# Optimization experiments

Hardware: AMD Instinct MI355X
Metric: run time of the kernel (lower is better)

The kernel has to match this reference:

```python
import jax, jax.numpy as jnp
import numpy as np

DIM, HEADS = 1024, 16
HEAD_DIM = DIM // HEADS
SCALE = HEAD_DIM ** -0.5


def setup_inputs() -> dict:
    key = jax.random.key(0)
    ks = jax.random.split(key, 5)
    B, N = 2, 2048
    x = jax.random.normal(ks[0], (B, N, DIM), dtype=jnp.float32)
    freqs = jax.random.normal(ks[1], (N, HEAD_DIM // 2), dtype=jnp.float32)
    w_qkv = jax.random.normal(ks[2], (3 * DIM, DIM), dtype=jnp.float32) * 0.02
    w_proj = jax.random.normal(ks[3], (DIM, DIM), dtype=jnp.float32) * 0.02
    b_proj = jnp.zeros((DIM,), dtype=jnp.float32)
    return {"x": x, "freqs": freqs, "w_qkv": w_qkv, "w_proj": w_proj, "b_proj": b_proj}


def _apply_rotary(t, cos, sin):
    # t: (B,N,H,D); cos/sin: (1,N,1,D//2)
    B, N, H, D = t.shape
    tp = t.reshape(B, N, H, D // 2, 2)
    x1, x2 = tp[..., 0], tp[..., 1]
    out = jnp.stack([x1 * cos - x2 * sin, x1 * sin + x2 * cos], axis=-1)
    return out.reshape(B, N, H, D)


def reference(x, freqs, w_qkv, w_proj, b_proj):
    B, N, C = x.shape
    H, D = HEADS, HEAD_DIM
    qkv = (x @ w_qkv.T).reshape(B, N, 3, H, D)  # fused QKV projection
    q, k, v = qkv[:, :, 0], qkv[:, :, 1], qkv[:, :, 2]  # each (B,N,H,D)
    cos = jnp.cos(freqs)[None, :, None, :]  # (1,N,1,D/2)
    sin = jnp.sin(freqs)[None, :, None, :]
    q = _apply_rotary(q, cos, sin)
    k = _apply_rotary(k, cos, sin)
    # SDPA: scores (B,H,N,N)
    scores = jnp.einsum("bqhd,bkhd->bhqk", q, k) * SCALE
    attn = jax.nn.softmax(scores, axis=-1)
    out = jnp.einsum("bhqk,bkhd->bqhd", attn, v).reshape(B, N, C)
    return out @ w_proj.T + b_proj
```

## Files before the change

### kernel.cpp

```cpp
#include <hip/hip_runtime.h>
#include <hip/hip_bf16.h>
#include <stdint.h>

#define BATCH   2
#define SEQ     2048
#define CDIM    1024
#define NHEAD   16
#define HDIM    64
#define MROWS   (BATCH*SEQ)
#define QKVN    (3*CDIM)
#define ATT_SCALE 0.125f

typedef __hip_bfloat16 bf16;
using bf16x8 = __attribute__((ext_vector_type(8))) __bf16;
using f32x4  = __attribute__((ext_vector_type(4))) float;

__device__ __forceinline__ void gld16(const void* g, void* l) {
    __builtin_amdgcn_global_load_lds(
        (__attribute__((address_space(1))) void*)(void*)(g),
        (__attribute__((address_space(3))) void*)(l),
        16, 0, 0);
}

__device__ __forceinline__ f32x4 mfma16x16x32(bf16x8 a, bf16x8 b, f32x4 c) {
    return __builtin_amdgcn_mfma_f32_16x16x32_bf16(a, b, c, 0, 0, 0);
}

__device__ __forceinline__ uint16_t bfbits(float v) {
    bf16 b = __float2bfloat16(v);
    return *(uint16_t*)&b;
}
__device__ __forceinline__ void store_out(bf16* p, float v) { *p = __float2bfloat16(v); }
__device__ __forceinline__ void store_out(float* p, float v) { *p = v; }

#define NX_F4 ((size_t)MROWS*CDIM/4)
#define NQ_F4 ((size_t)QKVN*CDIM/4)
#define NP_F4 ((size_t)CDIM*CDIM/4)
#define NF_SC ((size_t)SEQ*32)

__global__ __launch_bounds__(256)
void cvt_kernel(const float* __restrict__ x, const float* __restrict__ wq,
                const float* __restrict__ wp, const float* __restrict__ freqs,
                bf16* __restrict__ xb, bf16* __restrict__ wqb,
                bf16* __restrict__ wpb, float2* __restrict__ csn) {
    size_t i4 = (size_t)blockIdx.x*256 + threadIdx.x;
    if (i4 < NX_F4 + NQ_F4 + NP_F4) {
        const float* src; bf16* dst; size_t off;
        if (i4 < NX_F4)           { src = x;  dst = xb;  off = i4; }
        else if (i4 < NX_F4+NQ_F4){ src = wq; dst = wqb; off = i4 - NX_F4; }
        else                      { src = wp; dst = wpb; off = i4 - NX_F4 - NQ_F4; }
        float4 v = ((const float4*)src)[off];
        bf16 o[4] = { __float2bfloat16(v.x), __float2bfloat16(v.y),
                      __float2bfloat16(v.z), __float2bfloat16(v.w) };
        *(uint64_t*)(dst + off*4) = *(const uint64_t*)o;
    } else if (i4 < NX_F4 + NQ_F4 + NP_F4 + NF_SC) {
        size_t k = i4 - (NX_F4 + NQ_F4 + NP_F4);
        float f = freqs[k];
        csn[k] = make_float2(cosf(f), sinf(f));
    }
}

__global__ __launch_bounds__(256)
void gemm_qkv_rope(const bf16* __restrict__ A, const bf16* __restrict__ Bw,
                   const float2* __restrict__ csn, bf16* __restrict__ Qr,
                   bf16* __restrict__ Kr, bf16* __restrict__ VT) {
    const int K = CDIM, N = QKVN;
    __shared__ __align__(16) bf16 sh[64*136];
    bf16* As = sh;
    bf16* Bs = sh + 4096;

    const int bm = blockIdx.x, bn = blockIdx.y;
    const int tid  = threadIdx.x;
    const int lane = tid & 63;
    const int w    = tid >> 6;
    const int wm   = (w & 1) * 64;
    const int wn   = (w >> 1) * 64;
    const int quad = lane >> 4;
    const int l16  = lane & 15;

    const int c0 = tid, c1 = tid + 256;
    const size_t a_off0 = (size_t)(bm*128 + (c0 >> 2)) * K + (c0 & 3) * 8;
    const size_t a_off1 = (size_t)(bm*128 + (c1 >> 2)) * K + (c1 & 3) * 8;
    const size_t b_off0 = (size_t)(bn*128 + (c0 >> 2)) * K + (c0 & 3) * 8;
    const size_t b_off1 = (size_t)(bn*128 + (c1 >> 2)) * K + (c1 & 3) * 8;

    f32x4 acc[4][4] = {};

    for (int k0 = 0; k0 < K; k0 += 32) {
        __syncthreads();
        gld16(A + a_off0 + k0, &As[c0*8]);
        gld16(A + a_off1 + k0, &As[c1*8]);
        gld16(Bw + b_off0 + k0, &Bs[c0*8]);
        gld16(Bw + b_off1 + k0, &Bs[c1*8]);
        __syncthreads();

        bf16x8 af[4], bfv[4];
#pragma unroll
        for (int i = 0; i < 4; i++)
            af[i] = *(const bf16x8*)&As[(wm + i*16 + l16)*32 + quad*8];
#pragma unroll
        for (int i = 0; i < 4; i++)
            bfv[i] = *(const bf16x8*)&Bs[(wn + i*16 + l16)*32 + quad*8];
#pragma unroll
        for (int mi = 0; mi < 4; mi++)
#pragma unroll
            for (int ni = 0; ni < 4; ni++)
                acc[mi][ni] = mfma16x16x32(af[mi], bfv[ni], acc[mi][ni]);
    }

    const int region = bn >> 3;
    if (region < 2) {
        bf16* dst = region ? Kr : Qr;
        const int odd = l16 & 1;
#pragma unroll
        for (int mi = 0; mi < 4; mi++) {
#pragma unroll
            for (int ni = 0; ni < 4; ni++) {
                const int cq = (bn & 7)*128 + wn + ni*16 + l16;
                const int h = cq >> 6, d = cq & 63, fi = d >> 1;
#pragma unroll
                for (int r = 0; r < 4; r++) {
                    const int m = bm*128 + wm + mi*16 + quad*4 + r;
                    const int bb = m >> 11, n = m & 2047;
                    float own = acc[mi][ni][r];
                    float prt = __shfl_xor(own, 1);
                    float2 cs2 = csn[n*32 + fi];
                    float o = odd ? (prt*cs2.y + own*cs2.x)
                                  : (own*cs2.x - prt*cs2.y);
                    dst[((size_t)(bb*16 + h)*SEQ + n)*HDIM + d] = __float2bfloat16(o);
                }
            }
        }
    } else {
        const int bb = (bm*128) >> 11, n0 = (bm*128) & 2047;
        __syncthreads();
#pragma unroll
        for (int cc = 0; cc < 2; ++cc) {
            if ((w >> 1) == cc) {
#pragma unroll
                for (int mi = 0; mi < 4; mi++)
#pragma unroll
                    for (int ni = 0; ni < 4; ni++) {
                        const int d  = ni*16 + l16;
                        const int nl = wm + mi*16 + quad*4;
                        uint2 pk;
                        pk.x = (uint32_t)bfbits(acc[mi][ni][0]) |
                               ((uint32_t)bfbits(acc[mi][ni][1]) << 16);
                        pk.y = (uint32_t)bfbits(acc[mi][ni][2]) |
                               ((uint32_t)bfbits(acc[mi][ni][3]) << 16);
                        *(uint2*)&sh[d*136 + nl] = pk;
                    }
            }
            __syncthreads();
            const int h = (bn - 16)*2 + cc;
            const int d = tid >> 2, tn = tid & 3;
            bf16* vdst = VT + ((size_t)(bb*16 + h)*HDIM + d)*SEQ + n0 + tn*32;
#pragma unroll
            for (int j = 0; j < 4; j++)
                *(uint4*)(vdst + j*8) = *(const uint4*)&sh[d*136 + tn*32 + j*8];
            __syncthreads();
        }
    }
}

template<typename OutT, bool ADD_BIAS>
__global__ __launch_bounds__(256)
void gemm_bt(const bf16* __restrict__ A, const bf16* __restrict__ Bw,
             const float* __restrict__ bias, OutT* __restrict__ C,
             int M, int N, int K) {
    __shared__ __align__(16) bf16 As[128*32];
    __shared__ __align__(16) bf16 Bs[128*32];

    const int bm = blockIdx.x, bn = blockIdx.y;
    const int tid  = threadIdx.x;
    const int lane = tid & 63;
    const int w    = tid >> 6;
    const int wm   = (w & 1) * 64;
    const int wn   = (w >> 1) * 64;
    const int quad = lane >> 4;
    const int l16  = lane & 15;

    const int c0 = tid, c1 = tid + 256;
    const size_t a_off0 = (size_t)(bm*128 + (c0 >> 2)) * K + (c0 & 3) * 8;
    const size_t a_off1 = (size_t)(bm*128 + (c1 >> 2)) * K + (c1 & 3) * 8;
    const size_t b_off0 = (size_t)(bn*128 + (c0 >> 2)) * K + (c0 & 3) * 8;
    const size_t b_off1 = (size_t)(bn*128 + (c1 >> 2)) * K + (c1 & 3) * 8;

    f32x4 acc[4][4] = {};

    for (int k0 = 0; k0 < K; k0 += 32) {
        __syncthreads();
        gld16(A + a_off0 + k0, &As[c0*8]);
        gld16(A + a_off1 + k0, &As[c1*8]);
        gld16(Bw + b_off0 + k0, &Bs[c0*8]);
        gld16(Bw + b_off1 + k0, &Bs[c1*8]);
        __syncthreads();

        bf16x8 af[4], bfv[4];
#pragma unroll
        for (int i = 0; i < 4; i++)
            af[i] = *(const bf16x8*)&As[(wm + i*16 + l16)*32 + quad*8];
#pragma unroll
        for (int i = 0; i < 4; i++)
            bfv[i] = *(const bf16x8*)&Bs[(wn + i*16 + l16)*32 + quad*8];
#pragma unroll
        for (int mi = 0; mi < 4; mi++)
#pragma unroll
            for (int ni = 0; ni < 4; ni++)
                acc[mi][ni] = mfma16x16x32(af[mi], bfv[ni], acc[mi][ni]);
    }

#pragma unroll
    for (int mi = 0; mi < 4; mi++) {
        const int r0 = bm*128 + wm + mi*16 + quad*4;
#pragma unroll
        for (int ni = 0; ni < 4; ni++) {
            const int c = bn*128 + wn + ni*16 + l16;
            float bv = 0.f;
            if (ADD_BIAS) bv = bias[c];
#pragma unroll
            for (int r = 0; r < 4; r++)
                store_out(&C[(size_t)(r0 + r)*N + c], acc[mi][ni][r] + bv);
        }
    }
}

#define PSTRIDE 72

__global__ __launch_bounds__(256)
void attn_kernel(const bf16* __restrict__ Qr, const bf16* __restrict__ Kr,
                 const bf16* __restrict__ VT, bf16* __restrict__ Ao) {
    const int blk = blockIdx.x;
    const int bh  = blk >> 4;
    const int b   = bh >> 4, h = bh & 15;
    const int q0  = (blk & 15) * 128;
    const int tid = threadIdx.x;
    const int w   = tid >> 6, lane = tid & 63;
    const int quad = lane >> 4, l16 = lane & 15;

    __shared__ __align__(16) bf16 Ks[2][64*64];
    __shared__ __align__(16) bf16 Vs[2][64*64];
    __shared__ __align__(16) bf16 Ps[4][2*16*PSTRIDE];

    bf16x8 qf[2][2];
#pragma unroll
    for (int t = 0; t < 2; t++) {
        const int qrow = q0 + w*32 + t*16 + l16;
        const bf16* qp = Qr + ((size_t)bh*SEQ + qrow)*HDIM + quad*8;
        qf[t][0] = *(const bf16x8*)(qp);
        qf[t][1] = *(const bf16x8*)(qp + 32);
    }

    const int s0 = tid, s1 = tid + 256;
    const int r0 = s0 >> 3, g0 = (s0 & 7) ^ (r0 & 7);
    const int r1 = s1 >> 3, g1 = (s1 & 7) ^ (r1 & 7);
    const bf16* kb0 = Kr + (size_t)bh*SEQ*HDIM + r0*HDIM + g0*8;
    const bf16* kb1 = Kr + (size_t)bh*SEQ*HDIM + r1*HDIM + g1*8;
    const bf16* vb0 = VT + (size_t)bh*HDIM*SEQ + r0*SEQ + g0*8;
    const bf16* vb1 = VT + (size_t)bh*HDIM*SEQ + r1*SEQ + g1*8;

    f32x4 acc[2][4] = {};
    float lsum[2] = {0.f, 0.f};

    gld16(kb0, &Ks[0][s0*8]);
    gld16(kb1, &Ks[0][s1*8]);
    gld16(vb0, &Vs[0][s0*8]);
    gld16(vb1, &Vs[0][s1*8]);

    const int swz = l16 & 7;

    for (int it = 0; it < SEQ/64; ++it) {
        const int cur = it & 1, nxt = cur ^ 1;
        __syncthreads();
        if (it + 1 < SEQ/64) {
            const size_t ko = (size_t)(it + 1) * 64 * HDIM;
            const size_t vo = (size_t)(it + 1) * 64;
            gld16(kb0 + ko, &Ks[nxt][s0*8]);
            gld16(kb1 + ko, &Ks[nxt][s1*8]);
            gld16(vb0 + vo, &Vs[nxt][s0*8]);
            gld16(vb1 + vo, &Vs[nxt][s1*8]);
        }

        f32x4 sv[2][4];
#pragma unroll
        for (int j = 0; j < 4; j++) {
            const bf16* krow = &Ks[cur][(j*16 + l16)*64];
            bf16x8 ka = *(const bf16x8*)(krow + ((quad     ^ swz) * 8));
            bf16x8 kb = *(const bf16x8*)(krow + (((quad+4) ^ swz) * 8));
#pragma unroll
            for (int t = 0; t < 2; t++) {
                f32x4 tacc = {};
                tacc = mfma16x16x32(ka, qf[t][0], tacc);
                tacc = mfma16x16x32(kb, qf[t][1], tacc);
                sv[t][j] = tacc;
            }
        }

#pragma unroll
        for (int t = 0; t < 2; t++) {
#pragma unroll
            for (int j = 0; j < 4; j++) {
                float e0 = __expf(sv[t][j][0] * ATT_SCALE);
                float e1 = __expf(sv[t][j][1] * ATT_SCALE);
                float e2 = __expf(sv[t][j][2] * ATT_SCALE);
                float e3 = __expf(sv[t][j][3] * ATT_SCALE);
                lsum[t] += (e0 + e1) + (e2 + e3);
                uint2 pk;
                pk.x = (uint32_t)bfbits(e0) | ((uint32_t)bfbits(e1) << 16);
                pk.y = (uint32_t)bfbits(e2) | ((uint32_t)bfbits(e3) << 16);
                *(uint2*)&Ps[w][(t*16 + l16)*PSTRIDE + j*16 + quad*4] = pk;
            }
        }
        asm volatile("s_waitcnt lgkmcnt(0)" ::: "memory");

        bf16x8 pf[2][2];
#pragma unroll
        for (int t = 0; t < 2; t++) {
            const bf16* pr = &Ps[w][(t*16 + l16)*PSTRIDE + quad*8];
            pf[t][0] = *(const bf16x8*)(pr);
            pf[t][1] = *(const bf16x8*)(pr + 32);
        }
#pragma unroll
        for (int dt = 0; dt < 4; dt++) {
            const bf16* vrow = &Vs[cur][(dt*16 + l16)*64];
            bf16x8 va = *(const bf16x8*)(vrow + ((quad     ^ swz) * 8));
            bf16x8 vb = *(const bf16x8*)(vrow + (((quad+4) ^ swz) * 8));
#pragma unroll
            for (int t = 0; t < 2; t++) {
                acc[t][dt] = mfma16x16x32(pf[t][0], va, acc[t][dt]);
                acc[t][dt] = mfma16x16x32(pf[t][1], vb, acc[t][dt]);
            }
        }
    }

#pragma unroll
    for (int t = 0; t < 2; t++) {
        lsum[t] += __shfl_xor(lsum[t], 16, 64);
        lsum[t] += __shfl_xor(lsum[t], 32, 64);
    }
    float lt[2][4];
#pragma unroll
    for (int t = 0; t < 2; t++)
#pragma unroll
        for (int r = 0; r < 4; r++)
            lt[t][r] = __shfl(lsum[t], quad*20 + r, 64);

#pragma unroll
    for (int t = 0; t < 2; t++)
#pragma unroll
        for (int dt = 0; dt < 4; dt++)
#pragma unroll
            for (int r = 0; r < 4; r++) {
                int qr  = q0 + w*32 + t*16 + quad*4 + r;
                int col = h*HDIM + dt*16 + l16;
                Ao[(size_t)(b*SEQ + qr)*CDIM + col] =
                    __float2bfloat16(acc[t][dt][r] / lt[t][r]);
            }
}

extern "C" void kernel_launch(void* const* d_in, const int* in_sizes, int n_in,
                              void* d_out, int out_size, void* d_ws, size_t ws_size,
                              hipStream_t stream) {
    const float* x      = (const float*)d_in[0];
    const float* freqs  = (const float*)d_in[1];
    const float* w_qkv  = (const float*)d_in[2];
    const float* w_proj = (const float*)d_in[3];
    const float* b_proj = (const float*)d_in[4];
    float* out = (float*)d_out;

    char* ws = (char*)d_ws;
    bf16*   xb    = (bf16*)ws;   ws += (size_t)MROWS * CDIM * sizeof(bf16);
    bf16*   wqkvb = (bf16*)ws;   ws += (size_t)QKVN * CDIM * sizeof(bf16);
    bf16*   wprojb= (bf16*)ws;   ws += (size_t)CDIM * CDIM * sizeof(bf16);
    float2* csn   = (float2*)ws; ws += (size_t)SEQ * 32 * sizeof(float2);
    bf16*   Qr    = (bf16*)ws;   ws += (size_t)BATCH*NHEAD*SEQ*HDIM*sizeof(bf16);
    bf16*   Kr    = (bf16*)ws;   ws += (size_t)BATCH*NHEAD*SEQ*HDIM*sizeof(bf16);
    bf16*   VT    = (bf16*)ws;   ws += (size_t)BATCH*NHEAD*SEQ*HDIM*sizeof(bf16);
    bf16*   Ao    = (bf16*)ws;

    dim3 blk(256);
    {
        size_t nthr = NX_F4 + NQ_F4 + NP_F4 + NF_SC;
        cvt_kernel<<<dim3((nthr + 255) / 256), blk, 0, stream>>>(
            x, w_qkv, w_proj, freqs, xb, wqkvb, wprojb, csn);
    }
    gemm_qkv_rope<<<dim3(MROWS/128, QKVN/128), blk, 0, stream>>>(
        xb, wqkvb, csn, Qr, Kr, VT);
    attn_kernel<<<dim3(BATCH*NHEAD*(SEQ/128)), blk, 0, stream>>>(
        Qr, Kr, VT, Ao);
    gemm_bt<float, true><<<dim3(MROWS/128, CDIM/128), blk, 0, stream>>>(
        Ao, wprojb, b_proj, out, MROWS, CDIM, CDIM);
}
```

Measured before the change: 221.5 us.

## Keep softmax P in registers via 16x16x16 MFMA with pre-tiled V layout

The QKV GEMM epilogue now writes V in a fragment-tiled layout matching the 16x16x16 bf16 MFMA B-operand. This lets the attention kernel feed exponentiated scores straight from registers into the PV MFMAs instead of round-tripping P through shared memory. The softmax scale and log2(e) are folded into Q at projection time so exp2 can be used directly, and bf16 packing uses a cheap rounding bit trick. The trade-offs are twice as many (smaller) MFMA instructions for PV and a slightly different rounding scheme.

```diff
diff --git a/kernel.cpp b/kernel.cpp
--- a/kernel.cpp
+++ b/kernel.cpp
@@ -9,11 +9,12 @@
 #define HDIM    64
 #define MROWS   (BATCH*SEQ)
 #define QKVN    (3*CDIM)
-#define ATT_SCALE 0.125f
+#define QSCALE  0.18033688011112042f
 
 typedef __hip_bfloat16 bf16;
 using bf16x8 = __attribute__((ext_vector_type(8))) __bf16;
 using f32x4  = __attribute__((ext_vector_type(4))) float;
+using s16x4  = __attribute__((ext_vector_type(4))) short;
 
 __device__ __forceinline__ void gld16(const void* g, void* l) {
     __builtin_amdgcn_global_load_lds(
@@ -25,10 +26,18 @@
 __device__ __forceinline__ f32x4 mfma16x16x32(bf16x8 a, bf16x8 b, f32x4 c) {
     return __builtin_amdgcn_mfma_f32_16x16x32_bf16(a, b, c, 0, 0, 0);
 }
+__device__ __forceinline__ f32x4 mfma16x16x16(s16x4 a, s16x4 b, f32x4 c) {
+    return __builtin_amdgcn_mfma_f32_16x16x16bf16_1k(a, b, c, 0, 0, 0);
+}
 
 __device__ __forceinline__ uint16_t bfbits(float v) {
     bf16 b = __float2bfloat16(v);
     return *(uint16_t*)&b;
+}
+__device__ __forceinline__ uint32_t pkbf(float a, float b) {
+    uint32_t au = __builtin_bit_cast(uint32_t, a);
+    uint32_t bu = __builtin_bit_cast(uint32_t, b);
+    return ((au + 0x8000u) >> 16) | ((bu + 0x8000u) & 0xffff0000u);
 }
 __device__ __forceinline__ void store_out(bf16* p, float v) { *p = __float2bfloat16(v); }
 __device__ __forceinline__ void store_out(float* p, float v) { *p = v; }
@@ -63,8 +72,8 @@
 __global__ __launch_bounds__(256)
 void gemm_qkv_rope(const bf16* __restrict__ A, const bf16* __restrict__ Bw,
                    const float2* __restrict__ csn, bf16* __restrict__ Qr,
-                   bf16* __restrict__ Kr, bf16* __restrict__ VT) {
-    const int K = CDIM, N = QKVN;
+                   bf16* __restrict__ Kr, bf16* __restrict__ VG) {
+    const int K = CDIM;
     __shared__ __align__(16) bf16 sh[64*136];
     bf16* As = sh;
     bf16* Bs = sh + 4096;
@@ -111,6 +120,7 @@
     const int region = bn >> 3;
     if (region < 2) {
         bf16* dst = region ? Kr : Qr;
+        const float qs = region ? 1.0f : QSCALE;
         const int odd = l16 & 1;
 #pragma unroll
         for (int mi = 0; mi < 4; mi++) {
@@ -127,12 +137,13 @@
                     float2 cs2 = csn[n*32 + fi];
                     float o = odd ? (prt*cs2.y + own*cs2.x)
                                   : (own*cs2.x - prt*cs2.y);
-                    dst[((size_t)(bb*16 + h)*SEQ + n)*HDIM + d] = __float2bfloat16(o);
+                    dst[((size_t)(bb*16 + h)*SEQ + n)*HDIM + d] =
+                        __float2bfloat16(o * qs);
                 }
             }
         }
     } else {
-        const int bb = (bm*128) >> 11, n0 = (bm*128) & 2047;
+        const int bb = (bm*128) >> 11, n0l = (bm*128) & 2047;
         __syncthreads();
 #pragma unroll
         for (int cc = 0; cc < 2; ++cc) {
@@ -142,22 +153,30 @@
 #pragma unroll
                     for (int ni = 0; ni < 4; ni++) {
                         const int d  = ni*16 + l16;
-                        const int nl = wm + mi*16 + quad*4;
+                        const int tl = wm + mi*16 + quad*4;
                         uint2 pk;
                         pk.x = (uint32_t)bfbits(acc[mi][ni][0]) |
                                ((uint32_t)bfbits(acc[mi][ni][1]) << 16);
                         pk.y = (uint32_t)bfbits(acc[mi][ni][2]) |
                                ((uint32_t)bfbits(acc[mi][ni][3]) << 16);
-                        *(uint2*)&sh[d*136 + nl] = pk;
+                        *(uint2*)&sh[d*136 + tl] = pk;
                     }
             }
             __syncthreads();
             const int h = (bn - 16)*2 + cc;
-            const int d = tid >> 2, tn = tid & 3;
-            bf16* vdst = VT + ((size_t)(bb*16 + h)*HDIM + d)*SEQ + n0 + tn*32;
-#pragma unroll
-            for (int j = 0; j < 4; j++)
-                *(uint4*)(vdst + j*8) = *(const uint4*)&sh[d*136 + tn*32 + j*8];
+            bf16* vg = VG + (size_t)(bb*16 + h) * (SEQ*HDIM);
+#pragma unroll
+            for (int k = 0; k < 8; k++) {
+                int s8   = tid + 256*k;
+                int tile = s8 >> 10, si = s8 & 1023;
+                int g  = si >> 6,  ln = si & 63;
+                int j  = g >> 2,   dt = g & 3;
+                int qk = ln >> 4,  ld = ln & 15;
+                int tl = tile*64 + j*16 + qk*4;
+                int d  = dt*16 + ld;
+                *(uint2*)&vg[(size_t)((n0l >> 6) + tile)*4096 + si*4] =
+                    *(const uint2*)&sh[d*136 + tl];
+            }
             __syncthreads();
         }
     }
@@ -225,11 +244,9 @@
     }
 }
 
-#define PSTRIDE 72
-
 __global__ __launch_bounds__(256)
 void attn_kernel(const bf16* __restrict__ Qr, const bf16* __restrict__ Kr,
-                 const bf16* __restrict__ VT, bf16* __restrict__ Ao) {
+                 const bf16* __restrict__ VG, bf16* __restrict__ Ao) {
     const int blk = blockIdx.x;
     const int bh  = blk >> 4;
     const int b   = bh >> 4, h = bh & 15;
@@ -240,7 +257,6 @@
 
     __shared__ __align__(16) bf16 Ks[2][64*64];
     __shared__ __align__(16) bf16 Vs[2][64*64];
-    __shared__ __align__(16) bf16 Ps[4][2*16*PSTRIDE];
 
     bf16x8 qf[2][2];
 #pragma unroll
@@ -256,8 +272,9 @@
     const int r1 = s1 >> 3, g1 = (s1 & 7) ^ (r1 & 7);
     const bf16* kb0 = Kr + (size_t)bh*SEQ*HDIM + r0*HDIM + g0*8;
     const bf16* kb1 = Kr + (size_t)bh*SEQ*HDIM + r1*HDIM + g1*8;
-    const bf16* vb0 = VT + (size_t)bh*HDIM*SEQ + r0*SEQ + g0*8;
-    const bf16* vb1 = VT + (size_t)bh*HDIM*SEQ + r1*SEQ + g1*8;
+    const bf16* vgb = VG + (size_t)bh*SEQ*HDIM;
+    const bf16* vb0 = vgb + s0*8;
+    const bf16* vb1 = vgb + s1*8;
 
     f32x4 acc[2][4] = {};
     float lsum[2] = {0.f, 0.f};
@@ -273,12 +290,11 @@
         const int cur = it & 1, nxt = cur ^ 1;
         __syncthreads();
         if (it + 1 < SEQ/64) {
-            const size_t ko = (size_t)(it + 1) * 64 * HDIM;
-            const size_t vo = (size_t)(it + 1) * 64;
-            gld16(kb0 + ko, &Ks[nxt][s0*8]);
-            gld16(kb1 + ko, &Ks[nxt][s1*8]);
-            gld16(vb0 + vo, &Vs[nxt][s0*8]);
-            gld16(vb1 + vo, &Vs[nxt][s1*8]);
+            const size_t o = (size_t)(it + 1) * 4096;
+            gld16(kb0 + o, &Ks[nxt][s0*8]);
+            gld16(kb1 + o, &Ks[nxt][s1*8]);
+            gld16(vb0 + o, &Vs[nxt][s0*8]);
+            gld16(vb1 + o, &Vs[nxt][s1*8]);
         }
 
         f32x4 sv[2][4];
@@ -296,39 +312,30 @@
             }
         }
 
+        s16x4 pf[2][4];
 #pragma unroll
         for (int t = 0; t < 2; t++) {
 #pragma unroll
             for (int j = 0; j < 4; j++) {
-                float e0 = __expf(sv[t][j][0] * ATT_SCALE);
-                float e1 = __expf(sv[t][j][1] * ATT_SCALE);
-                float e2 = __expf(sv[t][j][2] * ATT_SCALE);
-                float e3 = __expf(sv[t][j][3] * ATT_SCALE);
+                float e0 = __builtin_amdgcn_exp2f(sv[t][j][0]);
+                float e1 = __builtin_amdgcn_exp2f(sv[t][j][1]);
+                float e2 = __builtin_amdgcn_exp2f(sv[t][j][2]);
+                float e3 = __builtin_amdgcn_exp2f(sv[t][j][3]);
                 lsum[t] += (e0 + e1) + (e2 + e3);
-                uint2 pk;
-                pk.x = (uint32_t)bfbits(e0) | ((uint32_t)bfbits(e1) << 16);
-                pk.y = (uint32_t)bfbits(e2) | ((uint32_t)bfbits(e3) << 16);
-                *(uint2*)&Ps[w][(t*16 + l16)*PSTRIDE + j*16 + quad*4] = pk;
-            }
-        }
-        asm volatile("s_waitcnt lgkmcnt(0)" ::: "memory");
-
-        bf16x8 pf[2][2];
-#pragma unroll
-        for (int t = 0; t < 2; t++) {
-            const bf16* pr = &Ps[w][(t*16 + l16)*PSTRIDE + quad*8];
-            pf[t][0] = *(const bf16x8*)(pr);
-            pf[t][1] = *(const bf16x8*)(pr + 32);
-        }
+                union { uint32_t u[2]; s16x4 v; } pa;
+                pa.u[0] = pkbf(e0, e1);
+                pa.u[1] = pkbf(e2, e3);
+                pf[t][j] = pa.v;
+            }
+        }
+
 #pragma unroll
         for (int dt = 0; dt < 4; dt++) {
-            const bf16* vrow = &Vs[cur][(dt*16 + l16)*64];
-            bf16x8 va = *(const bf16x8*)(vrow + ((quad     ^ swz) * 8));
-            bf16x8 vb = *(const bf16x8*)(vrow + (((quad+4) ^ swz) * 8));
-#pragma unroll
-            for (int t = 0; t < 2; t++) {
-                acc[t][dt] = mfma16x16x32(pf[t][0], va, acc[t][dt]);
-                acc[t][dt] = mfma16x16x32(pf[t][1], vb, acc[t][dt]);
+#pragma unroll
+            for (int j = 0; j < 4; j++) {
+                s16x4 vf = *(const s16x4*)&Vs[cur][((j*4 + dt)*64 + lane)*4];
+                acc[0][dt] = mfma16x16x16(pf[0][j], vf, acc[0][dt]);
+                acc[1][dt] = mfma16x16x16(pf[1][j], vf, acc[1][dt]);
             }
         }
     }
@@ -375,7 +382,7 @@
     float2* csn   = (float2*)ws; ws += (size_t)SEQ * 32 * sizeof(float2);
     bf16*   Qr    = (bf16*)ws;   ws += (size_t)BATCH*NHEAD*SEQ*HDIM*sizeof(bf16);
     bf16*   Kr    = (bf16*)ws;   ws += (size_t)BATCH*NHEAD*SEQ*HDIM*sizeof(bf16);
-    bf16*   VT    = (bf16*)ws;   ws += (size_t)BATCH*NHEAD*SEQ*HDIM*sizeof(bf16);
+    bf16*   VG    = (bf16*)ws;   ws += (size_t)BATCH*NHEAD*SEQ*HDIM*sizeof(bf16);
     bf16*   Ao    = (bf16*)ws;
 
     dim3 blk(256);
@@ -385,9 +392,9 @@
             x, w_qkv, w_proj, freqs, xb, wqkvb, wprojb, csn);
     }
     gemm_qkv_rope<<<dim3(MROWS/128, QKVN/128), blk, 0, stream>>>(
-        xb, wqkvb, csn, Qr, Kr, VT);
+        xb, wqkvb, csn, Qr, Kr, VG);
     attn_kernel<<<dim3(BATCH*NHEAD*(SEQ/128)), blk, 0, stream>>>(
-        Qr, Kr, VT, Ao);
+        Qr, Kr, VG, Ao);
     gemm_bt<float, true><<<dim3(MROWS/128, CDIM/128), blk, 0, stream>>>(
         Ao, wprojb, b_proj, out, MROWS, CDIM, CDIM);
 }
```

Result: faster. 212.6 us (-4.0%).
